# Performance work log

Measured on AMD Instinct MI355X. Metric: run time of the kernel, lower is better.

## Reference

```python
import jax, jax.numpy as jnp
import numpy as np

D_MODEL = 1024
NUM_HEADS = 16
D_K = D_MODEL // NUM_HEADS
B, S = 2, 2048


def setup_inputs() -> dict:
    key = jax.random.key(0)
    ks = jax.random.split(key, 11)
    sc = 1.0 / np.sqrt(D_MODEL)
    return {
        "query": jax.random.normal(ks[0], (B, S, D_MODEL), jnp.float32),
        "key": jax.random.normal(ks[1], (B, S, D_MODEL), jnp.float32),
        "value": jax.random.normal(ks[2], (B, S, D_MODEL), jnp.float32),
        "Wq": jax.random.normal(ks[3], (D_MODEL, D_MODEL), jnp.float32) * sc,
        "bq": jnp.zeros((D_MODEL,), jnp.float32),
        "Wk": jax.random.normal(ks[4], (D_MODEL, D_MODEL), jnp.float32) * sc,
        "bk": jnp.zeros((D_MODEL,), jnp.float32),
        "Wv": jax.random.normal(ks[5], (D_MODEL, D_MODEL), jnp.float32) * sc,
        "bv": jnp.zeros((D_MODEL,), jnp.float32),
        "Wo": jax.random.normal(ks[6], (D_MODEL, D_MODEL), jnp.float32) * sc,
        "bo": jnp.zeros((D_MODEL,), jnp.float32),
    }


def reference(query, key, value, Wq, bq, Wk, bk, Wv, bv, Wo, bo):
    b, sq, _ = query.shape
    # projections -> [B, H, S, d_k]
    def split_heads(x):
        return x.reshape(b, -1, NUM_HEADS, D_K).transpose(0, 2, 1, 3)

    q = split_heads(query @ Wq + bq)
    k = split_heads(key @ Wk + bk)
    v = split_heads(value @ Wv + bv)

    scores = jnp.einsum("bhqd,bhkd->bhqk", q, k) / np.sqrt(D_K).astype(np.float32)
    probs = jax.nn.softmax(scores, axis=-1)  # dropout p=0 (eval) -> identity
    attn = jnp.einsum("bhqk,bhkd->bhqd", probs, v)
    attn = attn.transpose(0, 2, 1, 3).reshape(b, sq, D_MODEL)
    out = attn @ Wo + bo
    return out, probs
```

## Files before the change

### kernel.cpp

```cpp
#include <hip/hip_runtime.h>


typedef __bf16 bf16x8 __attribute__((ext_vector_type(8)));
typedef float f32x4 __attribute__((ext_vector_type(4)));

typedef const unsigned int __attribute__((address_space(1))) as1c_uint;
typedef unsigned int __attribute__((address_space(3))) as3_uint;

#define S_LEN 2048
#define DM 1024
#define NH 16
#define DK 64
#define BATCH 2
#define M_ROWS 4096
#define KE 0.18033688f

__device__ __forceinline__ unsigned short f2bfu(float f) {
  union { __bf16 b; unsigned short u; } cv;
  cv.b = (__bf16)f;
  return cv.u;
}

__device__ __forceinline__ void gload_lds16(const void* g, void* l) {
  __builtin_amdgcn_global_load_lds((as1c_uint*)g, (as3_uint*)l, 16, 0, 0);
}

__global__ __launch_bounds__(256) void cvt3_kernel(
    const float* __restrict__ q, const float* __restrict__ k,
    const float* __restrict__ v, unsigned short* __restrict__ oq,
    unsigned short* __restrict__ ok_, unsigned short* __restrict__ ov) {
  const float* in = blockIdx.z == 0 ? q : (blockIdx.z == 1 ? k : v);
  unsigned short* out = blockIdx.z == 0 ? oq : (blockIdx.z == 1 ? ok_ : ov);
  size_t i = (size_t)blockIdx.x * 256 + threadIdx.x;
  float4 f = ((const float4*)in)[i];
  ushort4 u;
  u.x = f2bfu(f.x); u.y = f2bfu(f.y); u.z = f2bfu(f.z); u.w = f2bfu(f.w);
  ((ushort4*)out)[i] = u;
}

__global__ __launch_bounds__(256) void wtrans_kernel(
    const float* __restrict__ w0, const float* __restrict__ w1,
    const float* __restrict__ w2, const float* __restrict__ w3,
    unsigned short* __restrict__ o0, unsigned short* __restrict__ o1,
    unsigned short* __restrict__ o2, unsigned short* __restrict__ o3) {
  const float* W = blockIdx.z == 0 ? w0 : (blockIdx.z == 1 ? w1 : (blockIdx.z == 2 ? w2 : w3));
  unsigned short* WT = blockIdx.z == 0 ? o0 : (blockIdx.z == 1 ? o1 : (blockIdx.z == 2 ? o2 : o3));
  __shared__ float tile[32][33];
  int tx = threadIdx.x & 31, ty = threadIdx.x >> 5;
  int bx = blockIdx.x * 32, by = blockIdx.y * 32;
#pragma unroll
  for (int i = 0; i < 32; i += 8)
    tile[ty + i][tx] = W[(size_t)(by + ty + i) * DM + bx + tx];
  __syncthreads();
#pragma unroll
  for (int i = 0; i < 32; i += 8)
    WT[(size_t)(bx + ty + i) * DM + by + tx] = f2bfu(tile[tx][ty + i]);
}

template <int EPI>
__device__ __forceinline__ void gemm_core(const unsigned short* __restrict__ A,
                                          const unsigned short* __restrict__ BT,
                                          const float* __restrict__ bias,
                                          void* __restrict__ C) {
  __shared__ __attribute__((aligned(16))) unsigned short As[128 * 32];
  __shared__ __attribute__((aligned(16))) unsigned short Bs[128 * 32];
  const int tid = threadIdx.x;
  const int w = tid >> 6, l = tid & 63;
  const int wr = w >> 1, wc = w & 1;
  const int fr = l & 15, fq = l >> 4;
  const int m0 = blockIdx.y * 128, n0 = blockIdx.x * 128;
  const int srow = l >> 2;
  const int sk8 = (l & 3) * 8;
  f32x4 acc[4][4] = {};

  for (int k0 = 0; k0 < DM; k0 += 32) {
#pragma unroll
    for (int c = 0; c < 2; c++) {
      int r = c * 64 + w * 16;
      gload_lds16(A + (size_t)(m0 + r + srow) * DM + k0 + sk8, As + (size_t)r * 32);
      gload_lds16(BT + (size_t)(n0 + r + srow) * DM + k0 + sk8, Bs + (size_t)r * 32);
    }
    __syncthreads();
    bf16x8 af[4], bfv[4];
#pragma unroll
    for (int m = 0; m < 4; m++)
      af[m] = *(const bf16x8*)(As + (size_t)(wr * 64 + m * 16 + fr) * 32 + fq * 8);
#pragma unroll
    for (int n = 0; n < 4; n++)
      bfv[n] = *(const bf16x8*)(Bs + (size_t)(wc * 64 + n * 16 + fr) * 32 + fq * 8);
#pragma unroll
    for (int m = 0; m < 4; m++)
#pragma unroll
      for (int n = 0; n < 4; n++)
        acc[m][n] = __builtin_amdgcn_mfma_f32_16x16x32_bf16(af[m], bfv[n], acc[m][n], 0, 0, 0);
    __syncthreads();
  }

#pragma unroll
  for (int m = 0; m < 4; m++) {
#pragma unroll
    for (int n = 0; n < 4; n++) {
      const int col = n0 + wc * 64 + n * 16 + fr;
      const float bv = bias[col];
#pragma unroll
      for (int j = 0; j < 4; j++) {
        const int row = m0 + wr * 64 + m * 16 + fq * 4 + j;
        const float v = acc[m][n][j] + bv;
        if (EPI == 0) {
          ((float*)C)[(size_t)row * DM + col] = v;
        } else {
          const int b = row >> 11, s = row & (S_LEN - 1);
          const int h = col >> 6, d = col & (DK - 1);
          ((unsigned short*)C)[(((size_t)b * NH + h) * S_LEN + s) * DK + d] = f2bfu(v);
        }
      }
    }
  }
}

__global__ __launch_bounds__(256) void gemm_qkv_kernel(
    const unsigned short* __restrict__ xq, const unsigned short* __restrict__ xk,
    const unsigned short* __restrict__ xv, const unsigned short* __restrict__ wq,
    const unsigned short* __restrict__ wk, const unsigned short* __restrict__ wv,
    const float* __restrict__ bq, const float* __restrict__ bk,
    const float* __restrict__ bv, unsigned short* __restrict__ oq,
    unsigned short* __restrict__ okk, unsigned short* __restrict__ ov) {
  const int z = blockIdx.z;
  const unsigned short* A = z == 0 ? xq : (z == 1 ? xk : xv);
  const unsigned short* BT = z == 0 ? wq : (z == 1 ? wk : wv);
  const float* bias = z == 0 ? bq : (z == 1 ? bk : bv);
  unsigned short* C = z == 0 ? oq : (z == 1 ? okk : ov);
  gemm_core<1>(A, BT, bias, C);
}

__global__ __launch_bounds__(256) void gemm_out_kernel(
    const unsigned short* __restrict__ A, const unsigned short* __restrict__ BT,
    const float* __restrict__ bias, float* __restrict__ C) {
  gemm_core<0>(A, BT, bias, C);
}

__global__ __launch_bounds__(256) void vtrans_kernel(
    const unsigned short* __restrict__ V, unsigned short* __restrict__ VT) {
  __shared__ __attribute__((aligned(16))) unsigned short t[64][72];
  const int bh = blockIdx.y, s0 = blockIdx.x * 64;
  const unsigned short* v = V + ((size_t)bh * S_LEN + s0) * DK;
  const int tid = threadIdx.x;
#pragma unroll
  for (int i = 0; i < 4; i++) {
    int idx = tid + 256 * i;
    int r = idx >> 4, c4 = (idx & 15) * 4;
    *(ushort4*)&t[r][c4] = *(const ushort4*)(v + (size_t)r * DK + c4);
  }
  __syncthreads();
  unsigned short* o = VT + (size_t)bh * DK * S_LEN + s0;
#pragma unroll
  for (int i = 0; i < 4; i++) {
    int idx = tid + 256 * i;
    int d = idx >> 4, s4 = (idx & 15) * 4;
    ushort4 u;
    u.x = t[s4 + 0][d]; u.y = t[s4 + 1][d];
    u.z = t[s4 + 2][d]; u.w = t[s4 + 3][d];
    *(ushort4*)(o + (size_t)d * S_LEN + s4) = u;
  }
}

__global__ __launch_bounds__(256) void attn_kernel(
    const unsigned short* __restrict__ Qp, const unsigned short* __restrict__ Kp,
    const unsigned short* __restrict__ VT, float* __restrict__ probs,
    unsigned short* __restrict__ attnc) {
  const int flat = blockIdx.y * 32 + blockIdx.x;
  const int xcd = flat & 7, r = flat >> 3;
  const int bh = xcd * 4 + (r >> 5);
  const int tile = r & 31;
  const int w = threadIdx.x >> 6, l = threadIdx.x & 63;
  const int fr = l & 15, fq = l >> 4;
  const int q0 = tile * 64 + w * 16;
  const int qrow = q0 + fr;
  const unsigned short* Qh = Qp + (size_t)bh * S_LEN * DK;
  const unsigned short* Kh = Kp + (size_t)bh * S_LEN * DK;
  const unsigned short* Vh = VT + (size_t)bh * DK * S_LEN;
  float* ph = probs + (size_t)bh * S_LEN * S_LEN;

  __shared__ __attribute__((aligned(16))) unsigned short Kb[2][64 * 64];
  __shared__ __attribute__((aligned(16))) unsigned short Vb[2][64 * 64];
  __shared__ __attribute__((aligned(16))) unsigned short Pl[4][16][40];

  const int srow8 = l >> 3;
  const int sgran = ((l & 7) ^ (l >> 3)) << 3;
  const int kr7 = fr & 7;

  bf16x8 qf[2];
  qf[0] = *(const bf16x8*)(Qh + (size_t)qrow * DK + fq * 8);
  qf[1] = *(const bf16x8*)(Qh + (size_t)qrow * DK + 32 + fq * 8);

  float psum = 0.f;
#pragma unroll
  for (int i = 0; i < 2; i++)
    gload_lds16(Kh + (size_t)(w * 16 + i * 8 + srow8) * DK + sgran,
                &Kb[0][(w * 16 + i * 8) * 64]);
  asm volatile("s_waitcnt vmcnt(0)" : : : "memory");
  __builtin_amdgcn_s_barrier();
  for (int it = 0; it < S_LEN / 64; ++it) {
    const int cur = it & 1;
    if (it + 1 < S_LEN / 64) {
#pragma unroll
      for (int i = 0; i < 2; i++)
        gload_lds16(Kh + (size_t)((it + 1) * 64 + w * 16 + i * 8 + srow8) * DK + sgran,
                    &Kb[cur ^ 1][(w * 16 + i * 8) * 64]);
    }
#pragma unroll
    for (int t = 0; t < 4; t++) {
      const int rk = t * 16 + fr;
      const bf16x8 a0 = *(const bf16x8*)&Kb[cur][rk * 64 + ((fq ^ kr7) << 3)];
      const bf16x8 a1 = *(const bf16x8*)&Kb[cur][rk * 64 + (((fq + 4) ^ kr7) << 3)];
      f32x4 s4 = {0.f, 0.f, 0.f, 0.f};
      s4 = __builtin_amdgcn_mfma_f32_16x16x32_bf16(a0, qf[0], s4, 0, 0, 0);
      s4 = __builtin_amdgcn_mfma_f32_16x16x32_bf16(a1, qf[1], s4, 0, 0, 0);
#pragma unroll
      for (int j = 0; j < 4; j++) psum += __builtin_amdgcn_exp2f(s4[j] * KE);
    }
    if (it + 1 < S_LEN / 64) {
      asm volatile("s_waitcnt vmcnt(0)" : : : "memory");
      __builtin_amdgcn_s_barrier();
    }
  }
  psum += __shfl_xor(psum, 16, 64);
  psum += __shfl_xor(psum, 32, 64);
  const float pinv = 1.f / psum;

  f32x4 oacc[4] = {};
  float* phrow = ph + (size_t)qrow * S_LEN + fq * 4;
#pragma unroll
  for (int i = 0; i < 2; i++) {
    gload_lds16(Kh + (size_t)(w * 16 + i * 8 + srow8) * DK + sgran,
                &Kb[0][(w * 16 + i * 8) * 64]);
    gload_lds16(Vh + (size_t)(w * 16 + i * 8 + srow8) * S_LEN + sgran,
                &Vb[0][(w * 16 + i * 8) * 64]);
  }
  asm volatile("s_waitcnt vmcnt(0)" : : : "memory");
  __builtin_amdgcn_s_barrier();
  for (int it = 0; it < S_LEN / 64; ++it) {
    const int cur = it & 1;
    const int skb = it * 64;
    if (it + 1 < S_LEN / 64) {
#pragma unroll
      for (int i = 0; i < 2; i++) {
        gload_lds16(Kh + (size_t)(skb + 64 + w * 16 + i * 8 + srow8) * DK + sgran,
                    &Kb[cur ^ 1][(w * 16 + i * 8) * 64]);
        gload_lds16(Vh + (size_t)(w * 16 + i * 8 + srow8) * S_LEN + (skb + 64) + sgran,
                    &Vb[cur ^ 1][(w * 16 + i * 8) * 64]);
      }
    }
#pragma unroll
    for (int sub = 0; sub < 2; sub++) {
#pragma unroll
      for (int t = 0; t < 2; t++) {
        const int rk = sub * 32 + t * 16 + fr;
        const bf16x8 a0 = *(const bf16x8*)&Kb[cur][rk * 64 + ((fq ^ kr7) << 3)];
        const bf16x8 a1 = *(const bf16x8*)&Kb[cur][rk * 64 + (((fq + 4) ^ kr7) << 3)];
        f32x4 s4 = {0.f, 0.f, 0.f, 0.f};
        s4 = __builtin_amdgcn_mfma_f32_16x16x32_bf16(a0, qf[0], s4, 0, 0, 0);
        s4 = __builtin_amdgcn_mfma_f32_16x16x32_bf16(a1, qf[1], s4, 0, 0, 0);
        f32x4 pv;
        ushort4 pb;
#pragma unroll
        for (int j = 0; j < 4; j++) {
          const float p = __builtin_amdgcn_exp2f(s4[j] * KE) * pinv;
          pv[j] = p;
          ((unsigned short*)&pb)[j] = f2bfu(p);
        }
        __builtin_nontemporal_store(pv, (f32x4*)(phrow + skb + sub * 32 + t * 16));
        *(ushort4*)&Pl[w][fr][t * 16 + fq * 4] = pb;
      }
      const bf16x8 pa = *(const bf16x8*)&Pl[w][fr][fq * 8];
      __builtin_amdgcn_s_setprio(1);
#pragma unroll
      for (int n = 0; n < 4; n++) {
        const bf16x8 vf =
            *(const bf16x8*)&Vb[cur][(n * 16 + fr) * 64 + (((sub * 4 + fq) ^ kr7) << 3)];
        oacc[n] = __builtin_amdgcn_mfma_f32_16x16x32_bf16(pa, vf, oacc[n], 0, 0, 0);
      }
      __builtin_amdgcn_s_setprio(0);
    }
    if (it + 1 < S_LEN / 64) {
      asm volatile("s_waitcnt vmcnt(4)" : : : "memory");
      __builtin_amdgcn_s_barrier();
    }
  }

  const int b = bh >> 4, h = bh & (NH - 1);
#pragma unroll
  for (int n = 0; n < 4; n++) {
#pragma unroll
    for (int j = 0; j < 4; j++) {
      const int row = q0 + fq * 4 + j, col = h * DK + n * 16 + fr;
      attnc[(size_t)((size_t)b * S_LEN + row) * DM + col] = f2bfu(oacc[n][j]);
    }
  }
}

extern "C" void kernel_launch(void* const* d_in, const int* in_sizes, int n_in,
                              void* d_out, int out_size, void* d_ws, size_t ws_size,
                              hipStream_t stream) {
  const float* query = (const float*)d_in[0];
  const float* key   = (const float*)d_in[1];
  const float* value = (const float*)d_in[2];
  const float* Wq = (const float*)d_in[3];
  const float* bq = (const float*)d_in[4];
  const float* Wk = (const float*)d_in[5];
  const float* bk = (const float*)d_in[6];
  const float* Wv = (const float*)d_in[7];
  const float* bv = (const float*)d_in[8];
  const float* Wo = (const float*)d_in[9];
  const float* bo = (const float*)d_in[10];

  char* ws = (char*)d_ws;
  const size_t XSZ = (size_t)M_ROWS * DM * 2;
  const size_t WSZ = (size_t)DM * DM * 2;
  unsigned short* xq  = (unsigned short*)(ws);
  unsigned short* xk  = (unsigned short*)(ws + XSZ);
  unsigned short* xv  = (unsigned short*)(ws + 2 * XSZ);
  unsigned short* wtq = (unsigned short*)(ws + 3 * XSZ);
  unsigned short* wtk = (unsigned short*)(ws + 3 * XSZ + WSZ);
  unsigned short* wtv = (unsigned short*)(ws + 3 * XSZ + 2 * WSZ);
  unsigned short* wto = (unsigned short*)(ws + 3 * XSZ + 3 * WSZ);
  unsigned short* qp  = (unsigned short*)(ws + 3 * XSZ + 4 * WSZ);
  unsigned short* kp  = (unsigned short*)(ws + 4 * XSZ + 4 * WSZ);
  unsigned short* vp  = (unsigned short*)(ws + 5 * XSZ + 4 * WSZ);
  unsigned short* vT    = xk;
  unsigned short* attnc = xq;

  float* out = (float*)d_out;
  float* probs = (float*)d_out + (size_t)BATCH * S_LEN * DM;

  cvt3_kernel<<<dim3(4096, 1, 3), 256, 0, stream>>>(query, key, value, xq, xk, xv);
  wtrans_kernel<<<dim3(32, 32, 4), 256, 0, stream>>>(Wq, Wk, Wv, Wo, wtq, wtk, wtv, wto);
  gemm_qkv_kernel<<<dim3(8, 32, 3), 256, 0, stream>>>(xq, xk, xv, wtq, wtk, wtv,
                                                      bq, bk, bv, qp, kp, vp);
  vtrans_kernel<<<dim3(32, 32), 256, 0, stream>>>(vp, vT);
  attn_kernel<<<dim3(32, 32), 256, 0, stream>>>(qp, kp, vT, probs, attnc);
  gemm_out_kernel<<<dim3(8, 32), 256, 0, stream>>>(attnc, wto, bo, out);
}
```

Measured before the change: 281.5 us.

## Split softmax denominator pass into separate kernel with doubled Q rows per wave

Moves the first pass of attention (computing the row sums of exp(scores)) out of attn_kernel into a new psum_kernel. Each wave there handles two 16-row Q fragments, so every K tile staged into LDS is reused twice and the K traffic for this pass is halved. attn_kernel now reads the precomputed sums from a workspace buffer. The cost is an extra kernel launch, a small global round trip for the sums, and fewer blocks (512) in the psum pass, which may reduce occupancy.

```diff
diff --git a/kernel.cpp b/kernel.cpp
--- a/kernel.cpp
+++ b/kernel.cpp
@@ -164,10 +164,81 @@
   }
 }
 
+__global__ __launch_bounds__(256) void psum_kernel(
+    const unsigned short* __restrict__ Qp, const unsigned short* __restrict__ Kp,
+    float* __restrict__ psums) {
+  const int flat = blockIdx.x;
+  const int xcd = flat & 7, r = flat >> 3;
+  const int bh = xcd * 4 + (r >> 4);
+  const int tile = r & 15;
+  const int w = threadIdx.x >> 6, l = threadIdx.x & 63;
+  const int fr = l & 15, fq = l >> 4;
+  const int q0 = tile * 128 + w * 32;
+  const unsigned short* Qh = Qp + (size_t)bh * S_LEN * DK;
+  const unsigned short* Kh = Kp + (size_t)bh * S_LEN * DK;
+
+  __shared__ __attribute__((aligned(16))) unsigned short Kb[2][64 * 64];
+  const int srow8 = l >> 3;
+  const int sgran = ((l & 7) ^ (l >> 3)) << 3;
+  const int kr7 = fr & 7;
+
+  bf16x8 qf[2][2];
+#pragma unroll
+  for (int f = 0; f < 2; f++) {
+    qf[f][0] = *(const bf16x8*)(Qh + (size_t)(q0 + f * 16 + fr) * DK + fq * 8);
+    qf[f][1] = *(const bf16x8*)(Qh + (size_t)(q0 + f * 16 + fr) * DK + 32 + fq * 8);
+  }
+
+#define STAGE_KS(itn, buf)                                                    \
+  {                                                                           \
+    _Pragma("unroll") for (int i = 0; i < 2; i++)                             \
+        gload_lds16(Kh + (size_t)((itn) * 64 + w * 16 + i * 8 + srow8) * DK + \
+                        sgran,                                                \
+                    &Kb[buf][(w * 16 + i * 8) * 64]);                         \
+  }
+
+  float ps[2] = {0.f, 0.f};
+  STAGE_KS(0, 0);
+  asm volatile("s_waitcnt vmcnt(0)" : : : "memory");
+  __builtin_amdgcn_s_barrier();
+  for (int it = 0; it < S_LEN / 64; ++it) {
+    const int cur = it & 1;
+    if (it + 1 < S_LEN / 64) STAGE_KS(it + 1, cur ^ 1);
+#pragma unroll
+    for (int t = 0; t < 4; t++) {
+      const int rk = t * 16 + fr;
+      const bf16x8 a0 = *(const bf16x8*)&Kb[cur][rk * 64 + ((fq ^ kr7) << 3)];
+      const bf16x8 a1 = *(const bf16x8*)&Kb[cur][rk * 64 + (((fq + 4) ^ kr7) << 3)];
+#pragma unroll
+      for (int f = 0; f < 2; f++) {
+        f32x4 s4 = {0.f, 0.f, 0.f, 0.f};
+        s4 = __builtin_amdgcn_mfma_f32_16x16x32_bf16(a0, qf[f][0], s4, 0, 0, 0);
+        s4 = __builtin_amdgcn_mfma_f32_16x16x32_bf16(a1, qf[f][1], s4, 0, 0, 0);
+#pragma unroll
+        for (int j = 0; j < 4; j++) ps[f] += __builtin_amdgcn_exp2f(s4[j] * KE);
+      }
+    }
+    if (it + 1 < S_LEN / 64) {
+      asm volatile("s_waitcnt vmcnt(0)" : : : "memory");
+      __builtin_amdgcn_s_barrier();
+    }
+  }
+#pragma unroll
+  for (int f = 0; f < 2; f++) {
+    ps[f] += __shfl_xor(ps[f], 16, 64);
+    ps[f] += __shfl_xor(ps[f], 32, 64);
+  }
+  if (l < 16) {
+    psums[(size_t)bh * S_LEN + q0 + l] = ps[0];
+    psums[(size_t)bh * S_LEN + q0 + 16 + l] = ps[1];
+  }
+#undef STAGE_KS
+}
+
 __global__ __launch_bounds__(256) void attn_kernel(
     const unsigned short* __restrict__ Qp, const unsigned short* __restrict__ Kp,
-    const unsigned short* __restrict__ VT, float* __restrict__ probs,
-    unsigned short* __restrict__ attnc) {
+    const unsigned short* __restrict__ VT, const float* __restrict__ psums,
+    float* __restrict__ probs, unsigned short* __restrict__ attnc) {
   const int flat = blockIdx.y * 32 + blockIdx.x;
   const int xcd = flat & 7, r = flat >> 3;
   const int bh = xcd * 4 + (r >> 5);
@@ -189,44 +260,11 @@
   const int sgran = ((l & 7) ^ (l >> 3)) << 3;
   const int kr7 = fr & 7;
 
+  const float pinv = 1.f / psums[(size_t)bh * S_LEN + qrow];
+
   bf16x8 qf[2];
   qf[0] = *(const bf16x8*)(Qh + (size_t)qrow * DK + fq * 8);
   qf[1] = *(const bf16x8*)(Qh + (size_t)qrow * DK + 32 + fq * 8);
-
-  float psum = 0.f;
-#pragma unroll
-  for (int i = 0; i < 2; i++)
-    gload_lds16(Kh + (size_t)(w * 16 + i * 8 + srow8) * DK + sgran,
-                &Kb[0][(w * 16 + i * 8) * 64]);
-  asm volatile("s_waitcnt vmcnt(0)" : : : "memory");
-  __builtin_amdgcn_s_barrier();
-  for (int it = 0; it < S_LEN / 64; ++it) {
-    const int cur = it & 1;
-    if (it + 1 < S_LEN / 64) {
-#pragma unroll
-      for (int i = 0; i < 2; i++)
-        gload_lds16(Kh + (size_t)((it + 1) * 64 + w * 16 + i * 8 + srow8) * DK + sgran,
-                    &Kb[cur ^ 1][(w * 16 + i * 8) * 64]);
-    }
-#pragma unroll
-    for (int t = 0; t < 4; t++) {
-      const int rk = t * 16 + fr;
-      const bf16x8 a0 = *(const bf16x8*)&Kb[cur][rk * 64 + ((fq ^ kr7) << 3)];
-      const bf16x8 a1 = *(const bf16x8*)&Kb[cur][rk * 64 + (((fq + 4) ^ kr7) << 3)];
-      f32x4 s4 = {0.f, 0.f, 0.f, 0.f};
-      s4 = __builtin_amdgcn_mfma_f32_16x16x32_bf16(a0, qf[0], s4, 0, 0, 0);
-      s4 = __builtin_amdgcn_mfma_f32_16x16x32_bf16(a1, qf[1], s4, 0, 0, 0);
-#pragma unroll
-      for (int j = 0; j < 4; j++) psum += __builtin_amdgcn_exp2f(s4[j] * KE);
-    }
-    if (it + 1 < S_LEN / 64) {
-      asm volatile("s_waitcnt vmcnt(0)" : : : "memory");
-      __builtin_amdgcn_s_barrier();
-    }
-  }
-  psum += __shfl_xor(psum, 16, 64);
-  psum += __shfl_xor(psum, 32, 64);
-  const float pinv = 1.f / psum;
 
   f32x4 oacc[4] = {};
   float* phrow = ph + (size_t)qrow * S_LEN + fq * 4;
@@ -327,6 +365,7 @@
   unsigned short* qp  = (unsigned short*)(ws + 3 * XSZ + 4 * WSZ);
   unsigned short* kp  = (unsigned short*)(ws + 4 * XSZ + 4 * WSZ);
   unsigned short* vp  = (unsigned short*)(ws + 5 * XSZ + 4 * WSZ);
+  float*          psums = (float*)(ws + 6 * XSZ + 4 * WSZ);
   unsigned short* vT    = xk;
   unsigned short* attnc = xq;
 
@@ -338,6 +377,7 @@
   gemm_qkv_kernel<<<dim3(8, 32, 3), 256, 0, stream>>>(xq, xk, xv, wtq, wtk, wtv,
                                                       bq, bk, bv, qp, kp, vp);
   vtrans_kernel<<<dim3(32, 32), 256, 0, stream>>>(vp, vT);
-  attn_kernel<<<dim3(32, 32), 256, 0, stream>>>(qp, kp, vT, probs, attnc);
+  psum_kernel<<<dim3(512), 256, 0, stream>>>(qp, kp, psums);
+  attn_kernel<<<dim3(32, 32), 256, 0, stream>>>(qp, kp, vT, psums, probs, attnc);
   gemm_out_kernel<<<dim3(8, 32), 256, 0, stream>>>(attnc, wto, bo, out);
 }
```

Measured after the change: 298.1 us. 5.9% more time.
